# Kernel optimization log

Hardware: AMD Instinct MI355X
Metric: run time of the kernel (lower is better)

Reference implementation:

```python
import jax, jax.numpy as jnp
import numpy as np

ALPHA_1 = 0.5
ALPHA_2 = 0.9
TAU = 0.1
BIG_NUM = 1.0e9


def setup_inputs() -> dict:
    key = jax.random.key(0)
    k1, k2 = jax.random.split(key)
    B, N_SUP, N_QRY, D = 4, 512, 4096, 128
    features = jax.random.normal(k1, (B, N_SUP + N_QRY, D), dtype=jnp.float32)
    support_labels = jax.random.randint(k2, (B, N_SUP), 0, 64, dtype=jnp.int64)
    return {"features": features, "support_labels": support_labels}


def _sq_dists(x, y):
    # squared Euclidean pairwise distances: [B, N, M]
    xn = jnp.sum(x * x, axis=-1)  # [B, N]
    yn = jnp.sum(y * y, axis=-1)  # [B, M]
    xy = jnp.einsum('bnd,bmd->bnm', x, y)
    return xn[:, :, None] + yn[:, None, :] - 2.0 * xy


def reference(features, support_labels):
    n_support = support_labels.shape[1]
    support = features[:, :n_support]   # [B, S, D]
    query = features[:, n_support:]     # [B, Q, D]

    # --- re_represent_queries ---
    logits = -TAU * _sq_dists(query, query)           # [B, Q, Q]
    Q = query.shape[1]
    rng = jnp.arange(Q)
    logits = logits.at[:, rng, rng].set(-BIG_NUM)     # mask self-similarity
    attn_q = jax.nn.softmax(logits, axis=2)
    # Faithful to source: (attn[:,:,:,None] * q[:,:,None,:]).sum(2)
    # i.e. row index of q matches row index of attn; softmax axis j is contracted
    # against a broadcast copy of the same row.
    re_rep_q = jnp.einsum('bij,bid->bid', attn_q, query)
    new_query = (1.0 - ALPHA_1) * query + ALPHA_1 * re_rep_q

    # --- re_represent_supports ---
    logits_s = -TAU * _sq_dists(support, new_query)   # [B, S, Q]
    attn_s = jax.nn.softmax(logits_s, axis=2)
    re_rep_s = jnp.einsum('bsq,bqd->bsd', attn_s, new_query)
    new_support = (1.0 - ALPHA_2) * support + ALPHA_2 * re_rep_s

    return jnp.concatenate((new_support, new_query), axis=1)
```

## Files before the change

kernel.cpp:

```cpp
#include <hip/hip_runtime.h>

#define BATCH 4
#define NS 512
#define NQ 4096
#define D 128
#define NTOT (NS + NQ)

#define NCHUNK 16
#define QCHUNK (NQ / NCHUNK)
#define QT 64
#define ST 64
#define PITN 136
#define PITP 72

typedef __attribute__((ext_vector_type(8))) short bf16x8;
typedef __attribute__((ext_vector_type(4))) float f32x4;

#define L2E 1.4426950408889634f
#define SCL 0.28853900817779268f

__device__ __forceinline__ unsigned short f2bf(float f) {
    unsigned int x = __float_as_uint(f);
    return (unsigned short)((x + 0x7fffu + ((x >> 16) & 1u)) >> 16);
}

__device__ __forceinline__ unsigned int pk2(float a, float b) {
#if __has_builtin(__builtin_amdgcn_cvt_pk_bf16_f32)
    typedef __bf16 bf2 __attribute__((ext_vector_type(2)));
    bf2 r = __builtin_amdgcn_cvt_pk_bf16_f32(a, b);
    return __builtin_bit_cast(unsigned int, r);
#else
    return (unsigned)f2bf(a) | ((unsigned)f2bf(b) << 16);
#endif
}

__device__ __forceinline__ int qtIdx(int row, int col) {
    return ((row << 6) | col) ^ ((((row >> 3) ^ row) & 7) << 3);
}

__global__ __launch_bounds__(256) void attend_kernel(const float* __restrict__ feat,
                                                     float* __restrict__ out,
                                                     unsigned int* __restrict__ accPk,
                                                     float* __restrict__ lsumP) {
    __shared__ __align__(16) unsigned short qn_[QT * PITN];
    __shared__ __align__(16) unsigned short qt_[D * 64];
    __shared__ __align__(16) unsigned short p_[ST * PITP];
    __shared__ __align__(16) float qns[QCHUNK];

    int chunk = blockIdx.x, stile = blockIdx.y, b = blockIdx.z;
    int s0 = stile * ST;
    int q0 = chunk * QCHUNK;
    int t = threadIdx.x;
    int w = t >> 6, ln = t & 15, quad = (t >> 4) & 3;

    int qgrp = t >> 4;
    int qr0  = qgrp << 2;
    int dl   = t & 15;
    int d0   = dl << 3;

    const float* qchunk_base = feat + ((size_t)b * NTOT + NS + q0) * D;
    float* outq = out + ((size_t)b * NTOT + NS + q0) * D;

    float4 f0a, f0b, f1a, f1b, f2a, f2b, f3a, f3b;
    {
        const float* p = qchunk_base + (size_t)qr0 * D + d0;
        f0a = *(const float4*)p;           f0b = *(const float4*)(p + 4);
        f1a = *(const float4*)(p + D);     f1b = *(const float4*)(p + D + 4);
        f2a = *(const float4*)(p + 2 * D); f2b = *(const float4*)(p + 2 * D + 4);
        f3a = *(const float4*)(p + 3 * D); f3b = *(const float4*)(p + 3 * D + 4);
    }

    const float* srow = feat + ((size_t)b * NTOT + s0 + 16 * w + ln) * D;
    bf16x8 asup[4];
    #pragma unroll
    for (int kk = 0; kk < 4; ++kk) {
        float4 lo = *(const float4*)(srow + 32 * kk + 8 * quad);
        float4 hi = *(const float4*)(srow + 32 * kk + 8 * quad + 4);
        union { bf16x8 v; unsigned int u[4]; } pk;
        pk.u[0] = pk2(lo.x, lo.y);
        pk.u[1] = pk2(lo.z, lo.w);
        pk.u[2] = pk2(hi.x, hi.y);
        pk.u[3] = pk2(hi.z, hi.w);
        asup[kk] = pk.v;
    }

    f32x4 cpv[8];
    #pragma unroll
    for (int ds = 0; ds < 8; ++ds) cpv[ds] = (f32x4){0.f, 0.f, 0.f, 0.f};
    float lpart[4] = {0.f, 0.f, 0.f, 0.f};

    int copy_qt = (stile >> 1) << 6;
    int copy_ok = (qr0 >> 5) == (stile & 1);

    for (int qt = 0; qt < QCHUNK; qt += QT) {
        __syncthreads();

        int docopy = (qt == copy_qt) & copy_ok;
        float nr0, nr1, nr2, nr3;
        #define ROWW(r, va, vb) { \
            union { bf16x8 v; unsigned int u[4]; } pk; \
            pk.u[0] = pk2(va.x, va.y); pk.u[1] = pk2(va.z, va.w); \
            pk.u[2] = pk2(vb.x, vb.y); pk.u[3] = pk2(vb.z, vb.w); \
            *(bf16x8*)&qn_[(qr0 + r) * PITN + d0] = pk.v; \
            nr##r = va.x*va.x + va.y*va.y + va.z*va.z + va.w*va.w \
                  + vb.x*vb.x + vb.y*vb.y + vb.z*vb.z + vb.w*vb.w; \
            if (docopy) { \
                float* op = outq + (size_t)(qt + qr0 + r) * D + d0; \
                *(float4*)op = va; *(float4*)(op + 4) = vb; \
            } }
        ROWW(0, f0a, f0b)
        ROWW(1, f1a, f1b)
        ROWW(2, f2a, f2b)
        ROWW(3, f3a, f3b)
        #undef ROWW

        #define QTW(j, e0, e1, e2, e3) \
            *(uint2*)&qt_[qtIdx(d0 + j, qr0)] = make_uint2(pk2(e0, e1), pk2(e2, e3));
        QTW(0, f0a.x, f1a.x, f2a.x, f3a.x)
        QTW(1, f0a.y, f1a.y, f2a.y, f3a.y)
        QTW(2, f0a.z, f1a.z, f2a.z, f3a.z)
        QTW(3, f0a.w, f1a.w, f2a.w, f3a.w)
        QTW(4, f0b.x, f1b.x, f2b.x, f3b.x)
        QTW(5, f0b.y, f1b.y, f2b.y, f3b.y)
        QTW(6, f0b.z, f1b.z, f2b.z, f3b.z)
        QTW(7, f0b.w, f1b.w, f2b.w, f3b.w)
        #undef QTW

        #define RED4(x) x += __shfl_xor(x, 1, 64); x += __shfl_xor(x, 2, 64); \
                        x += __shfl_xor(x, 4, 64); x += __shfl_xor(x, 8, 64);
        RED4(nr0) RED4(nr1) RED4(nr2) RED4(nr3)
        #undef RED4
        if (dl == 0)
            *(float4*)&qns[qt + qr0] = make_float4(0.1f * L2E * nr0, 0.1f * L2E * nr1,
                                                   0.1f * L2E * nr2, 0.1f * L2E * nr3);
        __syncthreads();

        {
            int qtn = (qt + QT) & (QCHUNK - 1);
            const float* p = qchunk_base + (size_t)(qtn + qr0) * D + d0;
            f0a = *(const float4*)p;           f0b = *(const float4*)(p + 4);
            f1a = *(const float4*)(p + D);     f1b = *(const float4*)(p + D + 4);
            f2a = *(const float4*)(p + 2 * D); f2b = *(const float4*)(p + 2 * D + 4);
            f3a = *(const float4*)(p + 3 * D); f3b = *(const float4*)(p + 3 * D + 4);
        }

        f32x4 cqk[4];
        #pragma unroll
        for (int f = 0; f < 4; ++f) cqk[f] = (f32x4){0.f, 0.f, 0.f, 0.f};
        #pragma unroll
        for (int kk = 0; kk < 4; ++kk) {
            #pragma unroll
            for (int f = 0; f < 4; ++f) {
                bf16x8 bq = *(const bf16x8*)&qn_[(16 * f + ln) * PITN + 32 * kk + 8 * quad];
                cqk[f] = __builtin_amdgcn_mfma_f32_16x16x32_bf16(asup[kk], bq, cqk[f], 0, 0, 0);
            }
        }

        #pragma unroll
        for (int f = 0; f < 4; ++f) {
            float qs = qns[qt + 16 * f + ln];
            #pragma unroll
            for (int r = 0; r < 4; r += 2) {
                float e0 = exp2f(SCL * cqk[f][r]     - qs);
                float e1 = exp2f(SCL * cqk[f][r + 1] - qs);
                lpart[r] += e0;
                lpart[r + 1] += e1;
                unsigned int pe = pk2(e0, e1);
                p_[(16 * w + 4 * quad + r)     * PITP + 16 * f + ln] = (unsigned short)pe;
                p_[(16 * w + 4 * quad + r + 1) * PITP + 16 * f + ln] = (unsigned short)(pe >> 16);
            }
        }

        #pragma unroll
        for (int kk = 0; kk < 2; ++kk) {
            bf16x8 ap = *(const bf16x8*)&p_[(16 * w + ln) * PITP + 32 * kk + 8 * quad];
            #pragma unroll
            for (int ds = 0; ds < 8; ++ds) {
                bf16x8 bv = *(const bf16x8*)&qt_[qtIdx(16 * ds + ln, 32 * kk + 8 * quad)];
                cpv[ds] = __builtin_amdgcn_mfma_f32_16x16x32_bf16(ap, bv, cpv[ds], 0, 0, 0);
            }
        }
    }

    int base = (chunk * BATCH + b) * NS + s0;
    #pragma unroll
    for (int r = 0; r < 4; ++r) {
        float v = lpart[r];
        v += __shfl_xor(v, 1, 64);
        v += __shfl_xor(v, 2, 64);
        v += __shfl_xor(v, 4, 64);
        v += __shfl_xor(v, 8, 64);
        if (ln == 0) lsumP[base + 16 * w + 4 * quad + r] = v;
    }
    #pragma unroll
    for (int ds = 0; ds < 4; ++ds)
        #pragma unroll
        for (int r = 0; r < 4; ++r)
            accPk[(size_t)(base + 16 * w + 4 * quad + r) * 64 + 16 * ds + ln] =
                pk2(cpv[ds][r], cpv[ds + 4][r]);
}

__global__ __launch_bounds__(256) void epi_kernel(const float* __restrict__ feat,
                                                  const unsigned int* __restrict__ accPk,
                                                  const float* __restrict__ lsumP,
                                                  float* __restrict__ out) {
    int wave = threadIdx.x >> 6;
    int lane = threadIdx.x & 63;
    int row = blockIdx.x * 4 + wave;
    int b = row >> 9;
    int s = row & (NS - 1);

    float l = 0.f, a0 = 0.f, a1 = 0.f;
    #pragma unroll 4
    for (int c = 0; c < NCHUNK; ++c) {
        int base = (c * BATCH + b) * NS + s;
        l += lsumP[base];
        unsigned int pw = accPk[(size_t)base * 64 + lane];
        a0 += __uint_as_float(pw << 16);
        a1 += __uint_as_float(pw & 0xffff0000u);
    }
    float inv = 0.9f / l;
    size_t fo = ((size_t)b * NTOT + s) * D;
    float s0v = feat[fo + lane];
    float s1v = feat[fo + lane + 64];
    out[fo + lane]      = 0.1f * s0v + a0 * inv;
    out[fo + lane + 64] = 0.1f * s1v + a1 * inv;
}

extern "C" void kernel_launch(void* const* d_in, const int* in_sizes, int n_in,
                              void* d_out, int out_size, void* d_ws, size_t ws_size,
                              hipStream_t stream) {
    const float* feat = (const float*)d_in[0];
    float* out = (float*)d_out;
    unsigned int* accPk = (unsigned int*)d_ws;
    float* lsumP = (float*)(accPk + (size_t)NCHUNK * BATCH * NS * 64);
    (void)in_sizes; (void)n_in; (void)out_size; (void)ws_size;

    attend_kernel<<<dim3(NCHUNK, NS / ST, BATCH), 256, 0, stream>>>(feat, out, accPk, lsumP);
    epi_kernel<<<BATCH * NS / 4, 256, 0, stream>>>(feat, accPk, lsumP, out);
}
```

Before: 81.83 us.

## Register-block two support tiles per wave and rebalance query chunking

Doubles the support tile per block to 128 rows, so each wave computes two 16-row M-tiles. The query and value B-fragments read from LDS are then reused across both MFMA chains. To keep the grid the same size, the number of query chunks doubles, which halves the query span per block and doubles the partial accumulators the epilogue must reduce. It also fully unrolls the now two-iteration query loop and adds a two-blocks-per-CU launch bound. In exchange it raises register pressure and the workspace traffic for partial results.

```diff
diff --git a/kernel.cpp b/kernel.cpp
--- a/kernel.cpp
+++ b/kernel.cpp
@@ -6,10 +6,10 @@
 #define D 128
 #define NTOT (NS + NQ)
 
-#define NCHUNK 16
+#define NCHUNK 32
 #define QCHUNK (NQ / NCHUNK)
 #define QT 64
-#define ST 64
+#define ST 128
 #define PITN 136
 #define PITP 72
 
@@ -38,10 +38,10 @@
     return ((row << 6) | col) ^ ((((row >> 3) ^ row) & 7) << 3);
 }
 
-__global__ __launch_bounds__(256) void attend_kernel(const float* __restrict__ feat,
-                                                     float* __restrict__ out,
-                                                     unsigned int* __restrict__ accPk,
-                                                     float* __restrict__ lsumP) {
+__global__ __launch_bounds__(256, 2) void attend_kernel(const float* __restrict__ feat,
+                                                        float* __restrict__ out,
+                                                        unsigned int* __restrict__ accPk,
+                                                        float* __restrict__ lsumP) {
     __shared__ __align__(16) unsigned short qn_[QT * PITN];
     __shared__ __align__(16) unsigned short qt_[D * 64];
     __shared__ __align__(16) unsigned short p_[ST * PITP];
@@ -70,28 +70,34 @@
         f3a = *(const float4*)(p + 3 * D); f3b = *(const float4*)(p + 3 * D + 4);
     }
 
-    const float* srow = feat + ((size_t)b * NTOT + s0 + 16 * w + ln) * D;
-    bf16x8 asup[4];
-    #pragma unroll
-    for (int kk = 0; kk < 4; ++kk) {
-        float4 lo = *(const float4*)(srow + 32 * kk + 8 * quad);
-        float4 hi = *(const float4*)(srow + 32 * kk + 8 * quad + 4);
-        union { bf16x8 v; unsigned int u[4]; } pk;
-        pk.u[0] = pk2(lo.x, lo.y);
-        pk.u[1] = pk2(lo.z, lo.w);
-        pk.u[2] = pk2(hi.x, hi.y);
-        pk.u[3] = pk2(hi.z, hi.w);
-        asup[kk] = pk.v;
-    }
-
-    f32x4 cpv[8];
-    #pragma unroll
-    for (int ds = 0; ds < 8; ++ds) cpv[ds] = (f32x4){0.f, 0.f, 0.f, 0.f};
-    float lpart[4] = {0.f, 0.f, 0.f, 0.f};
+    bf16x8 asup[2][4];
+    #pragma unroll
+    for (int mi = 0; mi < 2; ++mi) {
+        const float* srow = feat + ((size_t)b * NTOT + s0 + 32 * w + 16 * mi + ln) * D;
+        #pragma unroll
+        for (int kk = 0; kk < 4; ++kk) {
+            float4 lo = *(const float4*)(srow + 32 * kk + 8 * quad);
+            float4 hi = *(const float4*)(srow + 32 * kk + 8 * quad + 4);
+            union { bf16x8 v; unsigned int u[4]; } pk;
+            pk.u[0] = pk2(lo.x, lo.y);
+            pk.u[1] = pk2(lo.z, lo.w);
+            pk.u[2] = pk2(hi.x, hi.y);
+            pk.u[3] = pk2(hi.z, hi.w);
+            asup[mi][kk] = pk.v;
+        }
+    }
+
+    f32x4 cpv[2][8];
+    #pragma unroll
+    for (int mi = 0; mi < 2; ++mi)
+        #pragma unroll
+        for (int ds = 0; ds < 8; ++ds) cpv[mi][ds] = (f32x4){0.f, 0.f, 0.f, 0.f};
+    float lpart[2][4] = {{0.f, 0.f, 0.f, 0.f}, {0.f, 0.f, 0.f, 0.f}};
 
     int copy_qt = (stile >> 1) << 6;
     int copy_ok = (qr0 >> 5) == (stile & 1);
 
+    #pragma unroll
     for (int qt = 0; qt < QCHUNK; qt += QT) {
         __syncthreads();
 
@@ -135,24 +141,27 @@
                                                    0.1f * L2E * nr2, 0.1f * L2E * nr3);
         __syncthreads();
 
-        {
-            int qtn = (qt + QT) & (QCHUNK - 1);
-            const float* p = qchunk_base + (size_t)(qtn + qr0) * D + d0;
+        if (qt + QT < QCHUNK) {
+            const float* p = qchunk_base + (size_t)(qt + QT + qr0) * D + d0;
             f0a = *(const float4*)p;           f0b = *(const float4*)(p + 4);
             f1a = *(const float4*)(p + D);     f1b = *(const float4*)(p + D + 4);
             f2a = *(const float4*)(p + 2 * D); f2b = *(const float4*)(p + 2 * D + 4);
             f3a = *(const float4*)(p + 3 * D); f3b = *(const float4*)(p + 3 * D + 4);
         }
 
-        f32x4 cqk[4];
-        #pragma unroll
-        for (int f = 0; f < 4; ++f) cqk[f] = (f32x4){0.f, 0.f, 0.f, 0.f};
+        f32x4 cqk[2][4];
+        #pragma unroll
+        for (int mi = 0; mi < 2; ++mi)
+            #pragma unroll
+            for (int f = 0; f < 4; ++f) cqk[mi][f] = (f32x4){0.f, 0.f, 0.f, 0.f};
         #pragma unroll
         for (int kk = 0; kk < 4; ++kk) {
             #pragma unroll
             for (int f = 0; f < 4; ++f) {
                 bf16x8 bq = *(const bf16x8*)&qn_[(16 * f + ln) * PITN + 32 * kk + 8 * quad];
-                cqk[f] = __builtin_amdgcn_mfma_f32_16x16x32_bf16(asup[kk], bq, cqk[f], 0, 0, 0);
+                #pragma unroll
+                for (int mi = 0; mi < 2; ++mi)
+                    cqk[mi][f] = __builtin_amdgcn_mfma_f32_16x16x32_bf16(asup[mi][kk], bq, cqk[mi][f], 0, 0, 0);
             }
         }
 
@@ -160,44 +169,55 @@
         for (int f = 0; f < 4; ++f) {
             float qs = qns[qt + 16 * f + ln];
             #pragma unroll
-            for (int r = 0; r < 4; r += 2) {
-                float e0 = exp2f(SCL * cqk[f][r]     - qs);
-                float e1 = exp2f(SCL * cqk[f][r + 1] - qs);
-                lpart[r] += e0;
-                lpart[r + 1] += e1;
-                unsigned int pe = pk2(e0, e1);
-                p_[(16 * w + 4 * quad + r)     * PITP + 16 * f + ln] = (unsigned short)pe;
-                p_[(16 * w + 4 * quad + r + 1) * PITP + 16 * f + ln] = (unsigned short)(pe >> 16);
+            for (int mi = 0; mi < 2; ++mi) {
+                #pragma unroll
+                for (int r = 0; r < 4; r += 2) {
+                    float e0 = exp2f(SCL * cqk[mi][f][r]     - qs);
+                    float e1 = exp2f(SCL * cqk[mi][f][r + 1] - qs);
+                    lpart[mi][r] += e0;
+                    lpart[mi][r + 1] += e1;
+                    unsigned int pe = pk2(e0, e1);
+                    p_[(32 * w + 16 * mi + 4 * quad + r)     * PITP + 16 * f + ln] = (unsigned short)pe;
+                    p_[(32 * w + 16 * mi + 4 * quad + r + 1) * PITP + 16 * f + ln] = (unsigned short)(pe >> 16);
+                }
             }
         }
 
         #pragma unroll
         for (int kk = 0; kk < 2; ++kk) {
-            bf16x8 ap = *(const bf16x8*)&p_[(16 * w + ln) * PITP + 32 * kk + 8 * quad];
+            bf16x8 ap[2];
+            #pragma unroll
+            for (int mi = 0; mi < 2; ++mi)
+                ap[mi] = *(const bf16x8*)&p_[(32 * w + 16 * mi + ln) * PITP + 32 * kk + 8 * quad];
             #pragma unroll
             for (int ds = 0; ds < 8; ++ds) {
                 bf16x8 bv = *(const bf16x8*)&qt_[qtIdx(16 * ds + ln, 32 * kk + 8 * quad)];
-                cpv[ds] = __builtin_amdgcn_mfma_f32_16x16x32_bf16(ap, bv, cpv[ds], 0, 0, 0);
+                #pragma unroll
+                for (int mi = 0; mi < 2; ++mi)
+                    cpv[mi][ds] = __builtin_amdgcn_mfma_f32_16x16x32_bf16(ap[mi], bv, cpv[mi][ds], 0, 0, 0);
             }
         }
     }
 
     int base = (chunk * BATCH + b) * NS + s0;
     #pragma unroll
-    for (int r = 0; r < 4; ++r) {
-        float v = lpart[r];
-        v += __shfl_xor(v, 1, 64);
-        v += __shfl_xor(v, 2, 64);
-        v += __shfl_xor(v, 4, 64);
-        v += __shfl_xor(v, 8, 64);
-        if (ln == 0) lsumP[base + 16 * w + 4 * quad + r] = v;
-    }
-    #pragma unroll
-    for (int ds = 0; ds < 4; ++ds)
-        #pragma unroll
-        for (int r = 0; r < 4; ++r)
-            accPk[(size_t)(base + 16 * w + 4 * quad + r) * 64 + 16 * ds + ln] =
-                pk2(cpv[ds][r], cpv[ds + 4][r]);
+    for (int mi = 0; mi < 2; ++mi) {
+        #pragma unroll
+        for (int r = 0; r < 4; ++r) {
+            float v = lpart[mi][r];
+            v += __shfl_xor(v, 1, 64);
+            v += __shfl_xor(v, 2, 64);
+            v += __shfl_xor(v, 4, 64);
+            v += __shfl_xor(v, 8, 64);
+            if (ln == 0) lsumP[base + 32 * w + 16 * mi + 4 * quad + r] = v;
+        }
+        #pragma unroll
+        for (int ds = 0; ds < 4; ++ds)
+            #pragma unroll
+            for (int r = 0; r < 4; ++r)
+                accPk[(size_t)(base + 32 * w + 16 * mi + 4 * quad + r) * 64 + 16 * ds + ln] =
+                    pk2(cpv[mi][ds][r], cpv[mi][ds + 4][r]);
+    }
 }
 
 __global__ __launch_bounds__(256) void epi_kernel(const float* __restrict__ feat,
@@ -211,7 +231,7 @@
     int s = row & (NS - 1);
 
     float l = 0.f, a0 = 0.f, a1 = 0.f;
-    #pragma unroll 4
+    #pragma unroll 8
     for (int c = 0; c < NCHUNK; ++c) {
         int base = (c * BATCH + b) * NS + s;
         l += lsumP[base];
```

After: 82.88 us. No clear change (+1.3%).
